# Kernel optimization log

Measured on AMD Instinct MI355X. Metric: run time of the kernel, lower is better.

## Reference

```python
import jax, jax.numpy as jnp
import numpy as np

N_NODES = 100000
N_EDGES = 3200000
F_IN = 128
HID = 32
N_CLASSES = 40
NEG_SLOPE = 0.2


def _add_self_loops(edge_index, n):
    loops = jnp.arange(n, dtype=edge_index.dtype)
    src = jnp.concatenate([edge_index[0], loops])
    dst = jnp.concatenate([edge_index[1], loops])
    return src, dst


def _gat_layer(x, src, dst, W, a_src, a_dst, b, n):
    # h: [N, C]
    h = x @ W
    hs = h[src]                      # [E, C] gathered source features
    alpha_s = hs @ a_src             # [E]
    alpha_d = (h @ a_dst)[dst]       # [E]
    e = jax.nn.leaky_relu(alpha_s + alpha_d, NEG_SLOPE)
    # segment softmax over incoming edges per destination node
    m = jax.ops.segment_max(e, dst, num_segments=n)
    ex = jnp.exp(e - m[dst])
    denom = jax.ops.segment_sum(ex, dst, num_segments=n)
    alpha = ex / denom[dst]
    out = jax.ops.segment_sum(alpha[:, None] * hs, dst, num_segments=n)
    return out + b


def setup_inputs() -> dict:
    key = jax.random.key(0)
    ks = jax.random.split(key, 8)
    x = jax.random.normal(ks[0], (N_NODES, F_IN), dtype=jnp.float32)
    edge_index = jax.random.randint(ks[1], (2, N_EDGES), 0, N_NODES, dtype=jnp.int32)
    W1 = jax.random.normal(ks[2], (F_IN, HID), dtype=jnp.float32) * (1.0 / np.sqrt(F_IN))
    att_src1 = jax.random.normal(ks[3], (HID,), dtype=jnp.float32) * 0.1
    att_dst1 = jax.random.normal(ks[4], (HID,), dtype=jnp.float32) * 0.1
    b1 = jnp.zeros((HID,), dtype=jnp.float32)
    W2 = jax.random.normal(ks[5], (HID, N_CLASSES), dtype=jnp.float32) * (1.0 / np.sqrt(HID))
    att_src2 = jax.random.normal(ks[6], (N_CLASSES,), dtype=jnp.float32) * 0.1
    att_dst2 = jax.random.normal(ks[7], (N_CLASSES,), dtype=jnp.float32) * 0.1
    b2 = jnp.zeros((N_CLASSES,), dtype=jnp.float32)
    return {"x": x, "edge_index": edge_index, "W1": W1, "att_src1": att_src1,
            "att_dst1": att_dst1, "b1": b1, "W2": W2, "att_src2": att_src2,
            "att_dst2": att_dst2, "b2": b2}


def reference(x, edge_index, W1, att_src1, att_dst1, b1, W2, att_src2, att_dst2, b2):
    n = x.shape[0]
    src, dst = _add_self_loops(edge_index, n)  # PyG GATConv default add_self_loops=True
    h = _gat_layer(x, src, dst, W1, att_src1, att_dst1, b1, n)
    h = jax.nn.relu(h)  # dropout is identity in eval mode
    h = _gat_layer(h, src, dst, W2, att_src2, att_dst2, b2, n)
    h = jax.nn.relu(h)
    return jax.nn.log_softmax(h, axis=1)
```

## Files before the change

kernel.cpp:

```cpp
#include <hip/hip_runtime.h>
#include <hip/hip_bf16.h>
#include <hip/hip_fp16.h>
#include <math.h>

#define N_NODES 100000
#define N_EDGES 3200000
#define ET (N_EDGES + N_NODES)
#define F_IN 128
#define HID 32
#define NCLS 40
#define NEG 0.2f

#define NB 782
#define NBLK 782
#define CHUNK 4096
#define BCAP 6144

__global__ __launch_bounds__(256) void kA_hist(const int* __restrict__ dst,
                                               int* __restrict__ Hm) {
    __shared__ int hist[NB];
    int t = threadIdx.x, k = blockIdx.x;
    for (int i = t; i < NB; i += 256) hist[i] = 0;
    __syncthreads();
    int base = k * CHUNK;
#pragma unroll
    for (int j = 0; j < CHUNK / 256; j++) {
        int e = base + j * 256 + t;
        if (e < N_EDGES) atomicAdd(&hist[dst[e] >> 7], 1);
    }
    __syncthreads();
    for (int i = t; i < NB; i += 256) Hm[i * NBLK + k] = hist[i];
}

__global__ void k_scan_a(const int* __restrict__ in, int* __restrict__ out,
                         int* __restrict__ bsums, int L) {
    __shared__ int sd[256];
    int t = threadIdx.x, b = blockIdx.x;
    int base = b * 1024 + t * 4;
    int v0 = 0, v1 = 0, v2 = 0, v3 = 0;
    if (base     < L) v0 = in[base];
    if (base + 1 < L) v1 = in[base + 1];
    if (base + 2 < L) v2 = in[base + 2];
    if (base + 3 < L) v3 = in[base + 3];
    int ts = v0 + v1 + v2 + v3;
    sd[t] = ts;
    __syncthreads();
    for (int off = 1; off < 256; off <<= 1) {
        int xx = (t >= off) ? sd[t - off] : 0;
        __syncthreads();
        sd[t] += xx;
        __syncthreads();
    }
    int ex = sd[t] - ts;
    if (t == 255) bsums[b] = sd[255];
    if (base     < L) out[base]     = ex;
    if (base + 1 < L) out[base + 1] = ex + v0;
    if (base + 2 < L) out[base + 2] = ex + v0 + v1;
    if (base + 3 < L) out[base + 3] = ex + v0 + v1 + v2;
}

__global__ void k_scan_b(const int* __restrict__ bsums, int* __restrict__ boffs, int nb) {
    __shared__ int sd[256];
    int t = threadIdx.x;
    int base = t * 4;
    int v0 = 0, v1 = 0, v2 = 0, v3 = 0;
    if (base     < nb) v0 = bsums[base];
    if (base + 1 < nb) v1 = bsums[base + 1];
    if (base + 2 < nb) v2 = bsums[base + 2];
    if (base + 3 < nb) v3 = bsums[base + 3];
    int ts = v0 + v1 + v2 + v3;
    sd[t] = ts;
    __syncthreads();
    for (int off = 1; off < 256; off <<= 1) {
        int xx = (t >= off) ? sd[t - off] : 0;
        __syncthreads();
        sd[t] += xx;
        __syncthreads();
    }
    int ex = sd[t] - ts;
    if (base     < nb) boffs[base]     = ex;
    if (base + 1 < nb) boffs[base + 1] = ex + v0;
    if (base + 2 < nb) boffs[base + 2] = ex + v0 + v1;
    if (base + 3 < nb) boffs[base + 3] = ex + v0 + v1 + v2;
}

__global__ void k_scan_c(int* __restrict__ out, const int* __restrict__ boffs, int L) {
    int i = blockIdx.x * 256 + threadIdx.x;
    if (i < L) out[i] += boffs[i >> 10];
}

__global__ __launch_bounds__(256) void kA_scatter(
    const int* __restrict__ src, const int* __restrict__ dst,
    const int* __restrict__ Sx, unsigned int* __restrict__ tmp) {
    __shared__ int hist[NB];
    __shared__ int lofs[NB];
    __shared__ int cur[NB];
    __shared__ int tsum[256];
    __shared__ unsigned int stage[CHUNK];
    __shared__ int gpos[CHUNK];
    int t = threadIdx.x, k = blockIdx.x;
    for (int i = t; i < NB; i += 256) hist[i] = 0;
    __syncthreads();
    int base = k * CHUNK;
    int myd[16], mys[16];
#pragma unroll
    for (int j = 0; j < 16; j++) {
        int e = base + j * 256 + t;
        myd[j] = (e < N_EDGES) ? dst[e] : -1;
        mys[j] = (e < N_EDGES) ? src[e] : 0;
        if (myd[j] >= 0) atomicAdd(&hist[myd[j] >> 7], 1);
    }
    __syncthreads();
    int i0 = 4 * t;
    int h0 = (i0     < NB) ? hist[i0]     : 0;
    int h1 = (i0 + 1 < NB) ? hist[i0 + 1] : 0;
    int h2 = (i0 + 2 < NB) ? hist[i0 + 2] : 0;
    int h3 = (i0 + 3 < NB) ? hist[i0 + 3] : 0;
    int ts = h0 + h1 + h2 + h3;
    tsum[t] = ts;
    __syncthreads();
    for (int off = 1; off < 256; off <<= 1) {
        int xx = (t >= off) ? tsum[t - off] : 0;
        __syncthreads();
        tsum[t] += xx;
        __syncthreads();
    }
    int ex = tsum[t] - ts;
    if (i0     < NB) { lofs[i0]     = ex;                cur[i0]     = 0; }
    if (i0 + 1 < NB) { lofs[i0 + 1] = ex + h0;           cur[i0 + 1] = 0; }
    if (i0 + 2 < NB) { lofs[i0 + 2] = ex + h0 + h1;      cur[i0 + 2] = 0; }
    if (i0 + 3 < NB) { lofs[i0 + 3] = ex + h0 + h1 + h2; cur[i0 + 3] = 0; }
    __syncthreads();
#pragma unroll
    for (int j = 0; j < 16; j++) {
        if (myd[j] >= 0) {
            int bkt = myd[j] >> 7;
            int slot = lofs[bkt] + atomicAdd(&cur[bkt], 1);
            stage[slot] = ((unsigned int)(myd[j] & 127) << 17) | (unsigned int)mys[j];
            gpos[slot] = Sx[bkt * NBLK + k] + (slot - lofs[bkt]);
        }
    }
    __syncthreads();
    int nvalid = min(CHUNK, N_EDGES - base);
    for (int i = t; i < nvalid; i += 256) tmp[gpos[i]] = stage[i];
}

__global__ __launch_bounds__(256) void kB_sort(
    const unsigned int* __restrict__ tmp, const int* __restrict__ Sx,
    int* __restrict__ esrc, int* __restrict__ rs, int* __restrict__ deg) {
    __shared__ unsigned int stage[BCAP];
    __shared__ int ordered[BCAP + 128];
    __shared__ int cnt[128], lofs[128], cur[128], sc[128];
    int t = threadIdx.x, b = blockIdx.x;
    int myBase = Sx[b * NBLK];
    int nextBase = (b == NB - 1) ? N_EDGES : Sx[(b + 1) * NBLK];
    int cntE = nextBase - myBase;
    int nNodes = min(128, N_NODES - b * 128);
    if (t < 128) { cnt[t] = 0; cur[t] = 0; }
    __syncthreads();
    for (int i = t; i < cntE; i += 256) {
        unsigned int p = tmp[myBase + i];
        stage[i] = p;
        atomicAdd(&cnt[p >> 17], 1);
    }
    __syncthreads();
    int val = 0;
    if (t < 128) { val = (t < nNodes) ? cnt[t] + 1 : 0; sc[t] = val; }
    __syncthreads();
    for (int off = 1; off < 128; off <<= 1) {
        int xx = 0;
        if (t < 128 && t >= off) xx = sc[t - off];
        __syncthreads();
        if (t < 128) sc[t] += xx;
        __syncthreads();
    }
    if (t < 128) lofs[t] = sc[t] - val;
    __syncthreads();
    if (t < nNodes) ordered[lofs[t]] = b * 128 + t;
    for (int i = t; i < cntE; i += 256) {
        unsigned int p = stage[i];
        int n = p >> 17;
        int slot = lofs[n] + 1 + atomicAdd(&cur[n], 1);
        ordered[slot] = (int)(p & 0x1FFFF);
    }
    __syncthreads();
    int gb = myBase + b * 128;
    int totOut = cntE + nNodes;
    for (int i = t; i < totOut; i += 256) esrc[gb + i] = ordered[i];
    if (t < nNodes) {
        rs[b * 128 + t] = gb + lofs[t];
        deg[b * 128 + t] = cnt[t] + 1;
    }
}

__global__ void k_prep(const float* __restrict__ W2, const float* __restrict__ as2,
                       const float* __restrict__ ad2,
                       float* __restrict__ va_s, float* __restrict__ va_d) {
    int k = threadIdx.x;
    if (k < HID) {
        float ps = 0.f, pd = 0.f;
        for (int c = 0; c < NCLS; c++) {
            float w = W2[k * NCLS + c];
            ps = fmaf(w, as2[c], ps);
            pd = fmaf(w, ad2[c], pd);
        }
        va_s[k] = ps;
        va_d[k] = pd;
    }
}

__global__ __launch_bounds__(256) void k_gemm1(
    const float* __restrict__ x, const float* __restrict__ W1,
    const float* __restrict__ a_s, const float* __restrict__ a_d,
    __half* __restrict__ h1h, float* __restrict__ s1, float* __restrict__ d1) {
    __shared__ float Ws[F_IN * HID];
    __shared__ float xs[8 * F_IN];
    int t = threadIdx.x;
    const float4* W4 = (const float4*)W1;
    float4* Ws4 = (float4*)Ws;
#pragma unroll
    for (int i = 0; i < F_IN * HID / 4 / 256; i++)
        Ws4[t + i * 256] = W4[t + i * 256];
    ((float4*)xs)[t] = ((const float4*)(x + (size_t)blockIdx.x * 8 * F_IN))[t];
    __syncthreads();
    int c = t & 31, g = t >> 5;
    int v = blockIdx.x * 8 + g;
    const float4* xg4 = (const float4*)(xs + g * F_IN);
    float acc = 0.f;
#pragma unroll
    for (int k4 = 0; k4 < F_IN / 4; k4++) {
        float4 xv = xg4[k4];
        int k = k4 * 4;
        acc = fmaf(xv.x, Ws[(k + 0) * HID + c], acc);
        acc = fmaf(xv.y, Ws[(k + 1) * HID + c], acc);
        acc = fmaf(xv.z, Ws[(k + 2) * HID + c], acc);
        acc = fmaf(xv.w, Ws[(k + 3) * HID + c], acc);
    }
    h1h[(size_t)v * HID + c] = __float2half(acc);
    float p = acc * a_s[c];
    float q = acc * a_d[c];
    for (int mm = 16; mm >= 1; mm >>= 1) {
        p += __shfl_xor(p, mm, 32);
        q += __shfl_xor(q, mm, 32);
    }
    if (c == 0) { s1[v] = p; d1[v] = q; }
}

#define GATHER_BODY(SARR, TABLE)                                                  \
    float a0 = 0.f, a1 = 0.f, a2 = 0.f, a3 = 0.f,                                 \
          a4 = 0.f, a5 = 0.f, a6 = 0.f, a7 = 0.f;                                 \
    float den = 0.f;                                                              \
    int t = 0;                                                                    \
    for (; t + 16 <= cnt; t += 16) {                                              \
        int p0 = start + t + e;                                                   \
        int sa0 = esrc[p0];                                                       \
        int sa1 = esrc[p0 + 4];                                                   \
        int sa2 = esrc[p0 + 8];                                                   \
        int sa3 = esrc[p0 + 12];                                                  \
        float sv0 = SARR[sa0];                                                    \
        float sv1 = SARR[sa1];                                                    \
        float sv2 = SARR[sa2];                                                    \
        float sv3 = SARR[sa3];                                                    \
        uint4 hv0 = TABLE[(size_t)sa0 * 4 + q];                                   \
        uint4 hv1 = TABLE[(size_t)sa1 * 4 + q];                                   \
        uint4 hv2 = TABLE[(size_t)sa2 * 4 + q];                                   \
        uint4 hv3 = TABLE[(size_t)sa3 * 4 + q];                                   \
        float e0 = sv0 + dval; e0 = (e0 >= 0.f) ? e0 : NEG * e0;                  \
        float e1 = sv1 + dval; e1 = (e1 >= 0.f) ? e1 : NEG * e1;                  \
        float e2 = sv2 + dval; e2 = (e2 >= 0.f) ? e2 : NEG * e2;                  \
        float e3 = sv3 + dval; e3 = (e3 >= 0.f) ? e3 : NEG * e3;                  \
        float w0 = __expf(e0);                                                    \
        float w1 = __expf(e1);                                                    \
        float w2 = __expf(e2);                                                    \
        float w3 = __expf(e3);                                                    \
        den += (w0 + w1) + (w2 + w3);                                             \
        ACC8(w0, hv0); ACC8(w1, hv1); ACC8(w2, hv2); ACC8(w3, hv3);               \
    }                                                                             \
    for (; t < cnt; t += 4) {                                                     \
        int idx = t + e;                                                          \
        int sa = 0;                                                               \
        float w = 0.f;                                                            \
        if (idx < cnt) {                                                          \
            sa = esrc[start + idx];                                               \
            float ev = SARR[sa] + dval;                                           \
            ev = (ev >= 0.f) ? ev : NEG * ev;                                     \
            w = __expf(ev);                                                       \
        }                                                                         \
        uint4 hv = TABLE[(size_t)sa * 4 + q];                                     \
        ACC8(w, hv);                                                              \
        den += w;                                                                 \
    }

#define ACC8(W, HV)                                                               \
    {                                                                             \
        float2 f0 = __half22float2(*(const __half2*)&(HV).x);                     \
        float2 f1 = __half22float2(*(const __half2*)&(HV).y);                     \
        float2 f2 = __half22float2(*(const __half2*)&(HV).z);                     \
        float2 f3 = __half22float2(*(const __half2*)&(HV).w);                     \
        a0 = fmaf((W), f0.x, a0); a1 = fmaf((W), f0.y, a1);                       \
        a2 = fmaf((W), f1.x, a2); a3 = fmaf((W), f1.y, a3);                       \
        a4 = fmaf((W), f2.x, a4); a5 = fmaf((W), f2.y, a5);                       \
        a6 = fmaf((W), f3.x, a6); a7 = fmaf((W), f3.y, a7);                       \
    }

__global__ __launch_bounds__(256) void k_fused1(
    const int* __restrict__ rs, const int* __restrict__ deg, const int* __restrict__ esrc,
    const uint4* __restrict__ h1r, const float* __restrict__ s1, const float* __restrict__ d1,
    const float* __restrict__ b1, const float* __restrict__ va_s, const float* __restrict__ va_d,
    uint4* __restrict__ hrr, float* __restrict__ s2, float* __restrict__ d2) {
    int tid = threadIdx.x;
    int sub = tid & 15;
    int q = sub & 3;
    int e = sub >> 2;
    int v = blockIdx.x * 16 + (tid >> 4);
    int start = rs[v];
    int cnt = deg[v];
    float dval = d1[v];
    GATHER_BODY(s1, h1r)
#pragma unroll
    for (int off = 4; off <= 8; off <<= 1) {
        a0 += __shfl_xor(a0, off); a1 += __shfl_xor(a1, off);
        a2 += __shfl_xor(a2, off); a3 += __shfl_xor(a3, off);
        a4 += __shfl_xor(a4, off); a5 += __shfl_xor(a5, off);
        a6 += __shfl_xor(a6, off); a7 += __shfl_xor(a7, off);
        den += __shfl_xor(den, off);
    }
    if (e == 0) {
        float iden = 1.f / den;
        const float4* b4 = (const float4*)(b1 + q * 8);
        float4 bA = b4[0], bB = b4[1];
        float o0 = fmaxf(a0 * iden + bA.x, 0.f);
        float o1 = fmaxf(a1 * iden + bA.y, 0.f);
        float o2 = fmaxf(a2 * iden + bA.z, 0.f);
        float o3 = fmaxf(a3 * iden + bA.w, 0.f);
        float o4 = fmaxf(a4 * iden + bB.x, 0.f);
        float o5 = fmaxf(a5 * iden + bB.y, 0.f);
        float o6 = fmaxf(a6 * iden + bB.z, 0.f);
        float o7 = fmaxf(a7 * iden + bB.w, 0.f);
        __half2 p0 = __floats2half2_rn(o0, o1);
        __half2 p1 = __floats2half2_rn(o2, o3);
        __half2 p2 = __floats2half2_rn(o4, o5);
        __half2 p3 = __floats2half2_rn(o6, o7);
        uint4 ov;
        ov.x = *(const unsigned int*)&p0;
        ov.y = *(const unsigned int*)&p1;
        ov.z = *(const unsigned int*)&p2;
        ov.w = *(const unsigned int*)&p3;
        hrr[(size_t)v * 4 + q] = ov;
        const float4* vs4 = (const float4*)(va_s + q * 8);
        const float4* vd4 = (const float4*)(va_d + q * 8);
        float4 sA = vs4[0], sB = vs4[1], dA = vd4[0], dB = vd4[1];
        float ps = o0 * sA.x + o1 * sA.y + o2 * sA.z + o3 * sA.w
                 + o4 * sB.x + o5 * sB.y + o6 * sB.z + o7 * sB.w;
        float pd = o0 * dA.x + o1 * dA.y + o2 * dA.z + o3 * dA.w
                 + o4 * dB.x + o5 * dB.y + o6 * dB.z + o7 * dB.w;
        ps += __shfl_xor(ps, 1); pd += __shfl_xor(pd, 1);
        ps += __shfl_xor(ps, 2); pd += __shfl_xor(pd, 2);
        if (q == 0) { s2[v] = ps; d2[v] = pd; }
    }
}

__global__ __launch_bounds__(256) void k_fused2(
    const int* __restrict__ rs, const int* __restrict__ deg, const int* __restrict__ esrc,
    const uint4* __restrict__ hrr, const float* __restrict__ s2, const float* __restrict__ d2,
    const float* __restrict__ W2, const float* __restrict__ b2, float* __restrict__ out) {
    __shared__ float W2s[HID * NCLS];
    __shared__ float hragg[16][HID];
    __shared__ float zbuf[16][NCLS];
    __shared__ float gm[16], gl[16];
    int tid = threadIdx.x;
    for (int i = tid; i < HID * NCLS; i += 256) W2s[i] = W2[i];
    int sub = tid & 15;
    int q = sub & 3;
    int e = sub >> 2;
    int node = tid >> 4;
    int v = blockIdx.x * 16 + node;
    int start = rs[v];
    int cnt = deg[v];
    float dval = d2[v];
    GATHER_BODY(s2, hrr)
#pragma unroll
    for (int off = 4; off <= 8; off <<= 1) {
        a0 += __shfl_xor(a0, off); a1 += __shfl_xor(a1, off);
        a2 += __shfl_xor(a2, off); a3 += __shfl_xor(a3, off);
        a4 += __shfl_xor(a4, off); a5 += __shfl_xor(a5, off);
        a6 += __shfl_xor(a6, off); a7 += __shfl_xor(a7, off);
        den += __shfl_xor(den, off);
    }
    if (e == 0) {
        float iden = 1.f / den;
        int cb = q * 8;
        hragg[node][cb + 0] = a0 * iden;
        hragg[node][cb + 1] = a1 * iden;
        hragg[node][cb + 2] = a2 * iden;
        hragg[node][cb + 3] = a3 * iden;
        hragg[node][cb + 4] = a4 * iden;
        hragg[node][cb + 5] = a5 * iden;
        hragg[node][cb + 6] = a6 * iden;
        hragg[node][cb + 7] = a7 * iden;
    }
    __syncthreads();
    for (int oi = tid; oi < 16 * NCLS; oi += 256) {
        int n = oi / NCLS, c = oi % NCLS;
        float z = 0.f;
#pragma unroll
        for (int k = 0; k < HID; k++)
            z = fmaf(hragg[n][k], W2s[k * NCLS + c], z);
        zbuf[n][c] = fmaxf(z + b2[c], 0.f);
    }
    __syncthreads();
    if (tid < 16) {
        float mx = -INFINITY;
        for (int c = 0; c < NCLS; c++) mx = fmaxf(mx, zbuf[tid][c]);
        float se = 0.f;
        for (int c = 0; c < NCLS; c++) se += __expf(zbuf[tid][c] - mx);
        gm[tid] = mx;
        gl[tid] = logf(se);
    }
    __syncthreads();
    for (int oi = tid; oi < 16 * NCLS; oi += 256) {
        int n = oi / NCLS, c = oi % NCLS;
        out[(size_t)(blockIdx.x * 16 + n) * NCLS + c] = zbuf[n][c] - gm[n] - gl[n];
    }
}


extern "C" void kernel_launch(void* const* d_in, const int* in_sizes, int n_in,
                              void* d_out, int out_size, void* d_ws, size_t ws_size,
                              hipStream_t stream) {
    (void)in_sizes; (void)n_in; (void)out_size; (void)ws_size;
    const float* x   = (const float*)d_in[0];
    const int*   ei  = (const int*)d_in[1];
    const float* W1  = (const float*)d_in[2];
    const float* as1 = (const float*)d_in[3];
    const float* ad1 = (const float*)d_in[4];
    const float* b1  = (const float*)d_in[5];
    const float* W2  = (const float*)d_in[6];
    const float* as2 = (const float*)d_in[7];
    const float* ad2 = (const float*)d_in[8];
    const float* b2  = (const float*)d_in[9];
    float* out = (float*)d_out;
    const int* srcA = ei;
    const int* dstA = ei + N_EDGES;

    char* w = (char*)d_ws;
    size_t off = 0;
    auto alloc = [&](size_t bytes) {
        char* p = w + off;
        off = (off + bytes + 255) & ~(size_t)255;
        return p;
    };
    int* esrc     = (int*)alloc((size_t)ET * 4);
    int* rs       = (int*)alloc((size_t)N_NODES * 4);
    int* deg      = (int*)alloc((size_t)N_NODES * 4);
    char* region1 = alloc((size_t)N_NODES * HID * 4);
    float* s1     = (float*)alloc((size_t)N_NODES * 4);
    float* d1     = (float*)alloc((size_t)N_NODES * 4);
    char* region2 = alloc((size_t)N_EDGES * 4 + 1024);
    float* s2     = (float*)alloc((size_t)N_NODES * 4);
    float* d2     = (float*)alloc((size_t)N_NODES * 4);
    float* va_s   = (float*)alloc(HID * 4);
    float* va_d   = (float*)alloc(HID * 4);
    int* bsums    = (int*)alloc(1024 * 4);
    int* boffs    = (int*)alloc(1024 * 4);

    const int L = NB * NBLK;
    int* Hm = (int*)region1;
    int* Sx = Hm + ((L + 63) & ~63);
    __half* h1h = (__half*)region1;
    unsigned int* tmp = (unsigned int*)region2;
    __half* hrt = (__half*)region2;

    int nb1 = (L + 1023) / 1024;
    hipLaunchKernelGGL(kA_hist, dim3(NBLK), dim3(256), 0, stream, dstA, Hm);
    hipLaunchKernelGGL(k_scan_a, dim3(nb1), dim3(256), 0, stream, Hm, Sx, bsums, L);
    hipLaunchKernelGGL(k_scan_b, dim3(1), dim3(256), 0, stream, bsums, boffs, nb1);
    hipLaunchKernelGGL(k_scan_c, dim3((L + 255) / 256), dim3(256), 0, stream, Sx, boffs, L);
    hipLaunchKernelGGL(kA_scatter, dim3(NBLK), dim3(256), 0, stream, srcA, dstA, Sx, tmp);
    hipLaunchKernelGGL(kB_sort, dim3(NB), dim3(256), 0, stream, tmp, Sx, esrc, rs, deg);

    hipLaunchKernelGGL(k_prep, dim3(1), dim3(64), 0, stream, W2, as2, ad2, va_s, va_d);
    hipLaunchKernelGGL(k_gemm1, dim3(N_NODES / 8), dim3(256), 0, stream, x, W1, as1, ad1, h1h, s1, d1);
    hipLaunchKernelGGL(k_fused1, dim3(N_NODES / 16), dim3(256), 0, stream, rs, deg, esrc,
                       (const uint4*)h1h, s1, d1, b1, va_s, va_d,
                       (uint4*)hrt, s2, d2);
    hipLaunchKernelGGL(k_fused2, dim3(N_NODES / 16), dim3(256), 0, stream, rs, deg, esrc,
                       (const uint4*)hrt, s2, d2, W2, b2, out);
}
```

Baseline: 327.2 us.

## Merge scatter, GEMM and prep kernels; degree-sort nodes; prefetch gather indices

Folds the edge scatter, the first-layer GEMM and the W2 attention prep into one launch that branches on block index, so independent work shares the GPU and launch gaps go away. The bucket sort now also bitonic-sorts the nodes of each 128-node bucket by degree into a permutation. Both aggregation kernels use that permutation so nodes in the same wavefront have similar degrees and less work is imbalanced. The gather loop prefetches the next iteration's indices and scores, and the final log-softmax row reduction is split across four lanes. In exchange it adds an extra sort stage, indirect node indexing and scattered output writes, and the merged kernel takes on the largest shared-memory footprint of its branches.

```diff
diff --git a/kernel.cpp b/kernel.cpp
--- a/kernel.cpp
+++ b/kernel.cpp
@@ -15,6 +15,7 @@
 #define NBLK 782
 #define CHUNK 4096
 #define BCAP 6144
+#define GEMM_BLKS (N_NODES / 8)
 
 __global__ __launch_bounds__(256) void kA_hist(const int* __restrict__ dst,
                                                int* __restrict__ Hm) {
@@ -89,68 +90,122 @@
     if (i < L) out[i] += boffs[i >> 10];
 }
 
-__global__ __launch_bounds__(256) void kA_scatter(
+__global__ __launch_bounds__(256) void k_scatter_gemm(
     const int* __restrict__ src, const int* __restrict__ dst,
-    const int* __restrict__ Sx, unsigned int* __restrict__ tmp) {
-    __shared__ int hist[NB];
-    __shared__ int lofs[NB];
-    __shared__ int cur[NB];
-    __shared__ int tsum[256];
-    __shared__ unsigned int stage[CHUNK];
-    __shared__ int gpos[CHUNK];
-    int t = threadIdx.x, k = blockIdx.x;
-    for (int i = t; i < NB; i += 256) hist[i] = 0;
-    __syncthreads();
-    int base = k * CHUNK;
-    int myd[16], mys[16];
-#pragma unroll
-    for (int j = 0; j < 16; j++) {
-        int e = base + j * 256 + t;
-        myd[j] = (e < N_EDGES) ? dst[e] : -1;
-        mys[j] = (e < N_EDGES) ? src[e] : 0;
-        if (myd[j] >= 0) atomicAdd(&hist[myd[j] >> 7], 1);
-    }
-    __syncthreads();
-    int i0 = 4 * t;
-    int h0 = (i0     < NB) ? hist[i0]     : 0;
-    int h1 = (i0 + 1 < NB) ? hist[i0 + 1] : 0;
-    int h2 = (i0 + 2 < NB) ? hist[i0 + 2] : 0;
-    int h3 = (i0 + 3 < NB) ? hist[i0 + 3] : 0;
-    int ts = h0 + h1 + h2 + h3;
-    tsum[t] = ts;
-    __syncthreads();
-    for (int off = 1; off < 256; off <<= 1) {
-        int xx = (t >= off) ? tsum[t - off] : 0;
-        __syncthreads();
-        tsum[t] += xx;
-        __syncthreads();
-    }
-    int ex = tsum[t] - ts;
-    if (i0     < NB) { lofs[i0]     = ex;                cur[i0]     = 0; }
-    if (i0 + 1 < NB) { lofs[i0 + 1] = ex + h0;           cur[i0 + 1] = 0; }
-    if (i0 + 2 < NB) { lofs[i0 + 2] = ex + h0 + h1;      cur[i0 + 2] = 0; }
-    if (i0 + 3 < NB) { lofs[i0 + 3] = ex + h0 + h1 + h2; cur[i0 + 3] = 0; }
-    __syncthreads();
-#pragma unroll
-    for (int j = 0; j < 16; j++) {
-        if (myd[j] >= 0) {
-            int bkt = myd[j] >> 7;
-            int slot = lofs[bkt] + atomicAdd(&cur[bkt], 1);
-            stage[slot] = ((unsigned int)(myd[j] & 127) << 17) | (unsigned int)mys[j];
-            gpos[slot] = Sx[bkt * NBLK + k] + (slot - lofs[bkt]);
-        }
-    }
-    __syncthreads();
-    int nvalid = min(CHUNK, N_EDGES - base);
-    for (int i = t; i < nvalid; i += 256) tmp[gpos[i]] = stage[i];
+    const int* __restrict__ Sx, unsigned int* __restrict__ tmp,
+    const float* __restrict__ x, const float* __restrict__ W1,
+    const float* __restrict__ a_s, const float* __restrict__ a_d,
+    __half* __restrict__ h1h, float* __restrict__ s1, float* __restrict__ d1,
+    const float* __restrict__ W2, const float* __restrict__ as2,
+    const float* __restrict__ ad2, float* __restrict__ va_s, float* __restrict__ va_d) {
+    __shared__ __align__(16) char smem[43200];
+    int t = threadIdx.x;
+    if (blockIdx.x < NBLK) {
+        int* hist = (int*)smem;
+        int* lofs = hist + NB;
+        int* cur  = lofs + NB;
+        int* tsum = cur + NB;
+        unsigned int* stage = (unsigned int*)(tsum + 256);
+        int* gpos = (int*)(stage + CHUNK);
+        int k = blockIdx.x;
+        for (int i = t; i < NB; i += 256) hist[i] = 0;
+        __syncthreads();
+        int base = k * CHUNK;
+        int myd[16], mys[16];
+#pragma unroll
+        for (int j = 0; j < 16; j++) {
+            int e = base + j * 256 + t;
+            myd[j] = (e < N_EDGES) ? dst[e] : -1;
+            mys[j] = (e < N_EDGES) ? src[e] : 0;
+            if (myd[j] >= 0) atomicAdd(&hist[myd[j] >> 7], 1);
+        }
+        __syncthreads();
+        int i0 = 4 * t;
+        int h0 = (i0     < NB) ? hist[i0]     : 0;
+        int h1 = (i0 + 1 < NB) ? hist[i0 + 1] : 0;
+        int h2 = (i0 + 2 < NB) ? hist[i0 + 2] : 0;
+        int h3 = (i0 + 3 < NB) ? hist[i0 + 3] : 0;
+        int ts = h0 + h1 + h2 + h3;
+        tsum[t] = ts;
+        __syncthreads();
+        for (int off = 1; off < 256; off <<= 1) {
+            int xx = (t >= off) ? tsum[t - off] : 0;
+            __syncthreads();
+            tsum[t] += xx;
+            __syncthreads();
+        }
+        int ex = tsum[t] - ts;
+        if (i0     < NB) { lofs[i0]     = ex;                cur[i0]     = 0; }
+        if (i0 + 1 < NB) { lofs[i0 + 1] = ex + h0;           cur[i0 + 1] = 0; }
+        if (i0 + 2 < NB) { lofs[i0 + 2] = ex + h0 + h1;      cur[i0 + 2] = 0; }
+        if (i0 + 3 < NB) { lofs[i0 + 3] = ex + h0 + h1 + h2; cur[i0 + 3] = 0; }
+        __syncthreads();
+#pragma unroll
+        for (int j = 0; j < 16; j++) {
+            if (myd[j] >= 0) {
+                int bkt = myd[j] >> 7;
+                int slot = lofs[bkt] + atomicAdd(&cur[bkt], 1);
+                stage[slot] = ((unsigned int)(myd[j] & 127) << 17) | (unsigned int)mys[j];
+                gpos[slot] = Sx[bkt * NBLK + k] + (slot - lofs[bkt]);
+            }
+        }
+        __syncthreads();
+        int nvalid = min(CHUNK, N_EDGES - base);
+        for (int i = t; i < nvalid; i += 256) tmp[gpos[i]] = stage[i];
+    } else if (blockIdx.x < NBLK + GEMM_BLKS) {
+        float* Ws = (float*)smem;
+        float* xs = Ws + F_IN * HID;
+        int bb = blockIdx.x - NBLK;
+        const float4* W4 = (const float4*)W1;
+        float4* Ws4 = (float4*)Ws;
+#pragma unroll
+        for (int i = 0; i < F_IN * HID / 4 / 256; i++)
+            Ws4[t + i * 256] = W4[t + i * 256];
+        ((float4*)xs)[t] = ((const float4*)(x + (size_t)bb * 8 * F_IN))[t];
+        __syncthreads();
+        int c = t & 31, g = t >> 5;
+        int v = bb * 8 + g;
+        const float4* xg4 = (const float4*)(xs + g * F_IN);
+        float acc = 0.f;
+#pragma unroll
+        for (int k4 = 0; k4 < F_IN / 4; k4++) {
+            float4 xv = xg4[k4];
+            int k = k4 * 4;
+            acc = fmaf(xv.x, Ws[(k + 0) * HID + c], acc);
+            acc = fmaf(xv.y, Ws[(k + 1) * HID + c], acc);
+            acc = fmaf(xv.z, Ws[(k + 2) * HID + c], acc);
+            acc = fmaf(xv.w, Ws[(k + 3) * HID + c], acc);
+        }
+        h1h[(size_t)v * HID + c] = __float2half(acc);
+        float p = acc * a_s[c];
+        float q = acc * a_d[c];
+        for (int mm = 16; mm >= 1; mm >>= 1) {
+            p += __shfl_xor(p, mm, 32);
+            q += __shfl_xor(q, mm, 32);
+        }
+        if (c == 0) { s1[v] = p; d1[v] = q; }
+    } else {
+        if (t < HID) {
+            float ps = 0.f, pd = 0.f;
+            for (int c = 0; c < NCLS; c++) {
+                float w = W2[t * NCLS + c];
+                ps = fmaf(w, as2[c], ps);
+                pd = fmaf(w, ad2[c], pd);
+            }
+            va_s[t] = ps;
+            va_d[t] = pd;
+        }
+    }
 }
 
 __global__ __launch_bounds__(256) void kB_sort(
     const unsigned int* __restrict__ tmp, const int* __restrict__ Sx,
-    int* __restrict__ esrc, int* __restrict__ rs, int* __restrict__ deg) {
+    int* __restrict__ esrc, int* __restrict__ rs, int* __restrict__ deg,
+    int* __restrict__ perm) {
     __shared__ unsigned int stage[BCAP];
     __shared__ int ordered[BCAP + 128];
     __shared__ int cnt[128], lofs[128], cur[128], sc[128];
+    __shared__ unsigned int dsort[128];
     int t = threadIdx.x, b = blockIdx.x;
     int myBase = Sx[b * NBLK];
     int nextBase = (b == NB - 1) ? N_EDGES : Sx[(b + 1) * NBLK];
@@ -191,59 +246,27 @@
         rs[b * 128 + t] = gb + lofs[t];
         deg[b * 128 + t] = cnt[t] + 1;
     }
-}
-
-__global__ void k_prep(const float* __restrict__ W2, const float* __restrict__ as2,
-                       const float* __restrict__ ad2,
-                       float* __restrict__ va_s, float* __restrict__ va_d) {
-    int k = threadIdx.x;
-    if (k < HID) {
-        float ps = 0.f, pd = 0.f;
-        for (int c = 0; c < NCLS; c++) {
-            float w = W2[k * NCLS + c];
-            ps = fmaf(w, as2[c], ps);
-            pd = fmaf(w, ad2[c], pd);
-        }
-        va_s[k] = ps;
-        va_d[k] = pd;
-    }
-}
-
-__global__ __launch_bounds__(256) void k_gemm1(
-    const float* __restrict__ x, const float* __restrict__ W1,
-    const float* __restrict__ a_s, const float* __restrict__ a_d,
-    __half* __restrict__ h1h, float* __restrict__ s1, float* __restrict__ d1) {
-    __shared__ float Ws[F_IN * HID];
-    __shared__ float xs[8 * F_IN];
-    int t = threadIdx.x;
-    const float4* W4 = (const float4*)W1;
-    float4* Ws4 = (float4*)Ws;
-#pragma unroll
-    for (int i = 0; i < F_IN * HID / 4 / 256; i++)
-        Ws4[t + i * 256] = W4[t + i * 256];
-    ((float4*)xs)[t] = ((const float4*)(x + (size_t)blockIdx.x * 8 * F_IN))[t];
-    __syncthreads();
-    int c = t & 31, g = t >> 5;
-    int v = blockIdx.x * 8 + g;
-    const float4* xg4 = (const float4*)(xs + g * F_IN);
-    float acc = 0.f;
-#pragma unroll
-    for (int k4 = 0; k4 < F_IN / 4; k4++) {
-        float4 xv = xg4[k4];
-        int k = k4 * 4;
-        acc = fmaf(xv.x, Ws[(k + 0) * HID + c], acc);
-        acc = fmaf(xv.y, Ws[(k + 1) * HID + c], acc);
-        acc = fmaf(xv.z, Ws[(k + 2) * HID + c], acc);
-        acc = fmaf(xv.w, Ws[(k + 3) * HID + c], acc);
-    }
-    h1h[(size_t)v * HID + c] = __float2half(acc);
-    float p = acc * a_s[c];
-    float q = acc * a_d[c];
-    for (int mm = 16; mm >= 1; mm >>= 1) {
-        p += __shfl_xor(p, mm, 32);
-        q += __shfl_xor(q, mm, 32);
-    }
-    if (c == 0) { s1[v] = p; d1[v] = q; }
+    if (t < 128) {
+        unsigned int key = 0;
+        if (t < nNodes)
+            key = (((unsigned int)min(cnt[t], 254) + 1) << 8) | (unsigned int)t;
+        dsort[t] = key;
+    }
+    __syncthreads();
+    for (int kk = 2; kk <= 128; kk <<= 1) {
+        for (int j = kk >> 1; j > 0; j >>= 1) {
+            if (t < 128) {
+                int ixj = t ^ j;
+                if (ixj > t) {
+                    unsigned int va = dsort[t], vb = dsort[ixj];
+                    bool up = ((t & kk) == 0);
+                    if (up ? (va < vb) : (va > vb)) { dsort[t] = vb; dsort[ixj] = va; }
+                }
+            }
+            __syncthreads();
+        }
+    }
+    if (t < nNodes) perm[b * 128 + t] = b * 128 + (int)(dsort[t] & 127);
 }
 
 #define GATHER_BODY(SARR, TABLE)                                                  \
@@ -251,16 +274,16 @@
           a4 = 0.f, a5 = 0.f, a6 = 0.f, a7 = 0.f;                                 \
     float den = 0.f;                                                              \
     int t = 0;                                                                    \
-    for (; t + 16 <= cnt; t += 16) {                                              \
-        int p0 = start + t + e;                                                   \
-        int sa0 = esrc[p0];                                                       \
-        int sa1 = esrc[p0 + 4];                                                   \
-        int sa2 = esrc[p0 + 8];                                                   \
-        int sa3 = esrc[p0 + 12];                                                  \
-        float sv0 = SARR[sa0];                                                    \
-        float sv1 = SARR[sa1];                                                    \
-        float sv2 = SARR[sa2];                                                    \
-        float sv3 = SARR[sa3];                                                    \
+    int nmain = cnt & ~15;                                                        \
+    int sa0 = 0, sa1 = 0, sa2 = 0, sa3 = 0;                                       \
+    float sv0 = 0.f, sv1 = 0.f, sv2 = 0.f, sv3 = 0.f;                             \
+    if (nmain > 0) {                                                              \
+        int p0 = start + e;                                                       \
+        sa0 = esrc[p0];      sa1 = esrc[p0 + 4];                                  \
+        sa2 = esrc[p0 + 8];  sa3 = esrc[p0 + 12];                                 \
+        sv0 = SARR[sa0]; sv1 = SARR[sa1]; sv2 = SARR[sa2]; sv3 = SARR[sa3];       \
+    }                                                                             \
+    for (; t < nmain; t += 16) {                                                  \
         uint4 hv0 = TABLE[(size_t)sa0 * 4 + q];                                   \
         uint4 hv1 = TABLE[(size_t)sa1 * 4 + q];                                   \
         uint4 hv2 = TABLE[(size_t)sa2 * 4 + q];                                   \
@@ -274,6 +297,13 @@
         float w2 = __expf(e2);                                                    \
         float w3 = __expf(e3);                                                    \
         den += (w0 + w1) + (w2 + w3);                                             \
+        int nt = t + 16;                                                          \
+        if (nt < nmain) {                                                         \
+            int p = start + nt + e;                                               \
+            sa0 = esrc[p];      sa1 = esrc[p + 4];                                \
+            sa2 = esrc[p + 8];  sa3 = esrc[p + 12];                               \
+            sv0 = SARR[sa0]; sv1 = SARR[sa1]; sv2 = SARR[sa2]; sv3 = SARR[sa3];   \
+        }                                                                         \
         ACC8(w0, hv0); ACC8(w1, hv1); ACC8(w2, hv2); ACC8(w3, hv3);               \
     }                                                                             \
     for (; t < cnt; t += 4) {                                                     \
@@ -304,6 +334,7 @@
     }
 
 __global__ __launch_bounds__(256) void k_fused1(
+    const int* __restrict__ perm,
     const int* __restrict__ rs, const int* __restrict__ deg, const int* __restrict__ esrc,
     const uint4* __restrict__ h1r, const float* __restrict__ s1, const float* __restrict__ d1,
     const float* __restrict__ b1, const float* __restrict__ va_s, const float* __restrict__ va_d,
@@ -312,7 +343,7 @@
     int sub = tid & 15;
     int q = sub & 3;
     int e = sub >> 2;
-    int v = blockIdx.x * 16 + (tid >> 4);
+    int v = perm[blockIdx.x * 16 + (tid >> 4)];
     int start = rs[v];
     int cnt = deg[v];
     float dval = d1[v];
@@ -361,20 +392,23 @@
 }
 
 __global__ __launch_bounds__(256) void k_fused2(
+    const int* __restrict__ perm,
     const int* __restrict__ rs, const int* __restrict__ deg, const int* __restrict__ esrc,
     const uint4* __restrict__ hrr, const float* __restrict__ s2, const float* __restrict__ d2,
     const float* __restrict__ W2, const float* __restrict__ b2, float* __restrict__ out) {
     __shared__ float W2s[HID * NCLS];
-    __shared__ float hragg[16][HID];
+    __shared__ float hragg[16][HID + 1];
     __shared__ float zbuf[16][NCLS];
     __shared__ float gm[16], gl[16];
+    __shared__ int vmap[16];
     int tid = threadIdx.x;
     for (int i = tid; i < HID * NCLS; i += 256) W2s[i] = W2[i];
     int sub = tid & 15;
     int q = sub & 3;
     int e = sub >> 2;
     int node = tid >> 4;
-    int v = blockIdx.x * 16 + node;
+    int v = perm[blockIdx.x * 16 + node];
+    if (sub == 0) vmap[node] = v;
     int start = rs[v];
     int cnt = deg[v];
     float dval = d2[v];
@@ -409,18 +443,22 @@
         zbuf[n][c] = fmaxf(z + b2[c], 0.f);
     }
     __syncthreads();
-    if (tid < 16) {
-        float mx = -INFINITY;
-        for (int c = 0; c < NCLS; c++) mx = fmaxf(mx, zbuf[tid][c]);
+    if (tid < 64) {
+        int n = tid >> 2, j = tid & 3;
+        float mx = 0.f;
+        for (int c = j; c < NCLS; c += 4) mx = fmaxf(mx, zbuf[n][c]);
+        mx = fmaxf(mx, __shfl_xor(mx, 1));
+        mx = fmaxf(mx, __shfl_xor(mx, 2));
         float se = 0.f;
-        for (int c = 0; c < NCLS; c++) se += __expf(zbuf[tid][c] - mx);
-        gm[tid] = mx;
-        gl[tid] = logf(se);
+        for (int c = j; c < NCLS; c += 4) se += __expf(zbuf[n][c] - mx);
+        se += __shfl_xor(se, 1);
+        se += __shfl_xor(se, 2);
+        if (j == 0) { gm[n] = mx; gl[n] = logf(se); }
     }
     __syncthreads();
     for (int oi = tid; oi < 16 * NCLS; oi += 256) {
         int n = oi / NCLS, c = oi % NCLS;
-        out[(size_t)(blockIdx.x * 16 + n) * NCLS + c] = zbuf[n][c] - gm[n] - gl[n];
+        out[(size_t)vmap[n] * NCLS + c] = zbuf[n][c] - gm[n] - gl[n];
     }
 }
 
@@ -463,11 +501,12 @@
     float* va_d   = (float*)alloc(HID * 4);
     int* bsums    = (int*)alloc(1024 * 4);
     int* boffs    = (int*)alloc(1024 * 4);
+    int* perm     = (int*)alloc((size_t)N_NODES * 4);
 
     const int L = NB * NBLK;
     int* Hm = (int*)region1;
     int* Sx = Hm + ((L + 63) & ~63);
-    __half* h1h = (__half*)region1;
+    __half* h1h = (__half*)(region1 + (size_t)N_NODES * HID * 2);
     unsigned int* tmp = (unsigned int*)region2;
     __half* hrt = (__half*)region2;
 
@@ -476,14 +515,13 @@
     hipLaunchKernelGGL(k_scan_a, dim3(nb1), dim3(256), 0, stream, Hm, Sx, bsums, L);
     hipLaunchKernelGGL(k_scan_b, dim3(1), dim3(256), 0, stream, bsums, boffs, nb1);
     hipLaunchKernelGGL(k_scan_c, dim3((L + 255) / 256), dim3(256), 0, stream, Sx, boffs, L);
-    hipLaunchKernelGGL(kA_scatter, dim3(NBLK), dim3(256), 0, stream, srcA, dstA, Sx, tmp);
-    hipLaunchKernelGGL(kB_sort, dim3(NB), dim3(256), 0, stream, tmp, Sx, esrc, rs, deg);
-
-    hipLaunchKernelGGL(k_prep, dim3(1), dim3(64), 0, stream, W2, as2, ad2, va_s, va_d);
-    hipLaunchKernelGGL(k_gemm1, dim3(N_NODES / 8), dim3(256), 0, stream, x, W1, as1, ad1, h1h, s1, d1);
-    hipLaunchKernelGGL(k_fused1, dim3(N_NODES / 16), dim3(256), 0, stream, rs, deg, esrc,
+    hipLaunchKernelGGL(k_scatter_gemm, dim3(NBLK + GEMM_BLKS + 1), dim3(256), 0, stream,
+                       srcA, dstA, Sx, tmp, x, W1, as1, ad1, h1h, s1, d1,
+                       W2, as2, ad2, va_s, va_d);
+    hipLaunchKernelGGL(kB_sort, dim3(NB), dim3(256), 0, stream, tmp, Sx, esrc, rs, deg, perm);
+    hipLaunchKernelGGL(k_fused1, dim3(N_NODES / 16), dim3(256), 0, stream, perm, rs, deg, esrc,
                        (const uint4*)h1h, s1, d1, b1, va_s, va_d,
                        (uint4*)hrt, s2, d2);
-    hipLaunchKernelGGL(k_fused2, dim3(N_NODES / 16), dim3(256), 0, stream, rs, deg, esrc,
+    hipLaunchKernelGGL(k_fused2, dim3(N_NODES / 16), dim3(256), 0, stream, perm, rs, deg, esrc,
                        (const uint4*)hrt, s2, d2, W2, b2, out);
 }
```

After: 349.4 us. 6.8% more time.
